# Performance work log

Measured on AMD Instinct MI355X. Metric: run time of the kernel, lower is better.

## Reference

```python
import jax, jax.numpy as jnp
import numpy as np


def grid_sample_bilinear(img, grid):
    """Replicates torch F.grid_sample(mode='bilinear', padding_mode='zeros',
    align_corners=False). img: [B,C,Hin,Win]; grid: [B,Ho,Wo,2] in [-1,1]
    with grid[...,0]=x (width), grid[...,1]=y (height). Returns [B,C,Ho,Wo]."""
    B, C, Hin, Win = img.shape
    x = (grid[..., 0] + 1.0) * (Win * 0.5) - 0.5  # unnormalized pixel coords
    y = (grid[..., 1] + 1.0) * (Hin * 0.5) - 0.5
    x0 = jnp.floor(x)
    y0 = jnp.floor(y)
    wx1 = x - x0
    wy1 = y - y0

    def tap(xi, yi, w):
        valid = ((xi >= 0) & (xi < Win) & (yi >= 0) & (yi < Hin)).astype(img.dtype)
        xc = jnp.clip(xi, 0, Win - 1).astype(jnp.int32)
        yc = jnp.clip(yi, 0, Hin - 1).astype(jnp.int32)
        def gather_one(im, yb, xb, wb):
            return im[:, yb, xb] * wb[None]  # [C,Ho,Wo]
        return jax.vmap(gather_one)(img, yc, xc, valid * w)

    return (tap(x0, y0, (1.0 - wx1) * (1.0 - wy1))
            + tap(x0 + 1.0, y0, wx1 * (1.0 - wy1))
            + tap(x0, y0 + 1.0, (1.0 - wx1) * wy1)
            + tap(x0 + 1.0, y0 + 1.0, wx1 * wy1))


def setup_inputs() -> dict:
    key = jax.random.key(0)
    k_uv, k1, k2, k3, k4 = jax.random.split(key, 5)
    W, H = 2048, 2048
    B, Ho, Wo = 8, 1024, 1024
    return {
        "uv": jax.random.uniform(k_uv, (B, Ho, Wo, 2), dtype=jnp.float32),
        "layer1": jax.random.normal(k1, (1, 1, W, H), dtype=jnp.float32),
        "layer2": jax.random.normal(k2, (1, 1, W // 2, H // 2), dtype=jnp.float32),
        "layer3": jax.random.normal(k3, (1, 1, W // 4, H // 4), dtype=jnp.float32),
        "layer4": jax.random.normal(k4, (1, 1, W // 8, H // 8), dtype=jnp.float32),
    }


def reference(uv, layer1, layer2, layer3, layer4):
    B = uv.shape[0]
    grid = uv * 2.0 - 1.0
    y = None
    for layer in (layer1, layer2, layer3, layer4):
        img = jnp.broadcast_to(layer, (B,) + layer.shape[1:])  # repeat(B,1,1,1)
        s = grid_sample_bilinear(img, grid)
        y = s if y is None else y + s
    return y  # [B,1,Ho,Wo]
```

## Files before the change

kernel.cpp:

```cpp
#include <hip/hip_runtime.h>
#include <hip/hip_fp16.h>


typedef unsigned int u32x2 __attribute__((ext_vector_type(2)));
typedef float f32x4 __attribute__((ext_vector_type(4)));

#define K 1024
#define CHUNK 4096
#define HB 4096
#define SEG (CHUNK * 256)
#define NXCD 8

__device__ __forceinline__ int binof(float u, float v) {
    int bx = min(max((int)(u * 32.0f), 0), 31);
    int by = min(max((int)(v * 32.0f), 0), 31);
    return by * 32 + bx;
}

__global__ __launch_bounds__(256) void repack_hist_kernel(
    const float* __restrict__ l1, const float* __restrict__ l2,
    const float* __restrict__ l3, const float* __restrict__ l4,
    __half2* __restrict__ r1, __half2* __restrict__ r2,
    __half2* __restrict__ r3, __half2* __restrict__ r4,
    const float2* __restrict__ uv, unsigned* __restrict__ hist, int n) {
    const int n1 = 2048 * 2048, n2 = 1024 * 1024, n3 = 512 * 512, n4 = 256 * 256;
    int i = blockIdx.x * 256 + threadIdx.x;
    {
        const float* __restrict__ src = nullptr;
        __half2* __restrict__ dst = nullptr;
        int S = 0, logS = 0, j = 0;
        if (i < n1) {
            src = l1; dst = r1; S = 2048; logS = 11; j = i;
        } else if (i < n1 + n2) {
            src = l2; dst = r2; S = 1024; logS = 10; j = i - n1;
        } else if (i < n1 + n2 + n3) {
            src = l3; dst = r3; S = 512; logS = 9; j = i - (n1 + n2);
        } else if (i < n1 + n2 + n3 + n4) {
            src = l4; dst = r4; S = 256; logS = 8; j = i - (n1 + n2 + n3);
        }
        if (src) {
            int y = j >> logS;
            float a = src[j];
            float b = src[(y < S - 1) ? (j + S) : j];
            dst[j] = __halves2half2(__float2half(a), __float2half(b));
        }
    }
    if (hist == nullptr) return;
    int base = blockIdx.x * HB;
    if (base >= n) return;
    __shared__ unsigned cnt[K];
    for (int b = threadIdx.x; b < K; b += 256) cnt[b] = 0u;
    __syncthreads();
    int m = min(HB, n - base);
    const f32x4* uv4 = (const f32x4*)(uv + base);
    int npair = m >> 1;
    for (int k2 = threadIdx.x; k2 < npair; k2 += 256) {
        f32x4 q = __builtin_nontemporal_load(&uv4[k2]);
        atomicAdd(&cnt[binof(q.x, q.y)], 1u);
        atomicAdd(&cnt[binof(q.z, q.w)], 1u);
    }
    if ((m & 1) && threadIdx.x == 0) {
        float2 q = uv[base + m - 1];
        atomicAdd(&cnt[binof(q.x, q.y)], 1u);
    }
    __syncthreads();
    int seg = base / SEG;
    unsigned* gh = hist + (size_t)seg * K;
    for (int b = threadIdx.x; b < K; b += 256) {
        unsigned v = cnt[b];
        if (v) atomicAdd(&gh[b], v);
    }
}

__global__ __launch_bounds__(256) void partition_kernel(
    const float2* __restrict__ uv, const unsigned* __restrict__ hist,
    unsigned* __restrict__ cursor, float2* __restrict__ uv_s,
    unsigned* __restrict__ idx_s, int n, int pinned) {
    __shared__ float2 suv[CHUNK];
    __shared__ unsigned short slid[CHUNK];
    __shared__ unsigned cnt[K];
    __shared__ unsigned lbase[K];
    __shared__ unsigned goff[K];
    __shared__ unsigned part[256];
    int t = threadIdx.x;
    int blk = blockIdx.x;
    int c = pinned ? ((blk % NXCD) * (SEG / CHUNK) + blk / NXCD) : blk;
    int cb = c * CHUNK;
    if (cb >= n) return;
    int cnum = min(CHUNK, n - cb);
    int seg = cb / SEG;
    unsigned segstart = (unsigned)((size_t)seg * SEG);

    {
        const f32x4* uv4 = (const f32x4*)(uv + cb);
        int npair = cnum >> 1;
        for (int k2 = t; k2 < npair; k2 += 256) {
            f32x4 q = uv4[k2];
            suv[k2 * 2] = make_float2(q.x, q.y);
            suv[k2 * 2 + 1] = make_float2(q.z, q.w);
        }
        if ((cnum & 1) && t == 0) suv[cnum - 1] = uv[cb + cnum - 1];
    }
    for (int b = t; b < K; b += 256) cnt[b] = 0u;
    __syncthreads();
    for (int k = t; k < cnum; k += 256)
        atomicAdd(&cnt[binof(suv[k].x, suv[k].y)], 1u);
    __syncthreads();
    {
        unsigned v0 = cnt[t * 4], v1 = cnt[t * 4 + 1], v2 = cnt[t * 4 + 2],
                 v3 = cnt[t * 4 + 3];
        unsigned s1 = v0, s2 = v0 + v1, s3 = v0 + v1 + v2;
        part[t] = s3 + v3;
        __syncthreads();
        for (int off = 1; off < 256; off <<= 1) {
            unsigned x = (t >= off) ? part[t - off] : 0u;
            __syncthreads();
            part[t] += x;
            __syncthreads();
        }
        unsigned tb = (t > 0) ? part[t - 1] : 0u;
        lbase[t * 4] = tb;
        lbase[t * 4 + 1] = tb + s1;
        lbase[t * 4 + 2] = tb + s2;
        lbase[t * 4 + 3] = tb + s3;
    }
    __syncthreads();
    {
        const unsigned* h = hist + (size_t)seg * K;
        unsigned v0 = h[t * 4], v1 = h[t * 4 + 1], v2 = h[t * 4 + 2],
                 v3 = h[t * 4 + 3];
        unsigned s1 = v0, s2 = v0 + v1, s3 = v0 + v1 + v2;
        part[t] = s3 + v3;
        __syncthreads();
        for (int off = 1; off < 256; off <<= 1) {
            unsigned x = (t >= off) ? part[t - off] : 0u;
            __syncthreads();
            part[t] += x;
            __syncthreads();
        }
        unsigned tb = (t > 0) ? part[t - 1] : 0u;
        unsigned sbv[4] = {tb, tb + s1, tb + s2, tb + s3};
        for (int j = 0; j < 4; ++j) {
            int b = t * 4 + j;
            unsigned cc = cnt[b];
            unsigned r = cc ? atomicAdd(&cursor[(size_t)seg * K + b], cc) : 0u;
            goff[b] = segstart + sbv[j] + r;
        }
    }
    __syncthreads();
    for (int b = t; b < K; b += 256) cnt[b] = 0u;
    __syncthreads();
    for (int k = t; k < cnum; k += 256) {
        int b = binof(suv[k].x, suv[k].y);
        unsigned r = lbase[b] + atomicAdd(&cnt[b], 1u);
        slid[r] = (unsigned short)k;
    }
    __syncthreads();
    for (int s = t; s < cnum; s += 256) {
        int lid = slid[s];
        float2 q = suv[lid];
        int b = binof(q.x, q.y);
        unsigned pos = goff[b] + ((unsigned)s - lbase[b]);
        uv_s[pos] = q;
        idx_s[pos] = (unsigned)(cb + lid);
    }
}

__device__ __forceinline__ float sample_level(const __half2* __restrict__ R,
                                              const int S, const float gx,
                                              const float gy) {
    const float halfS = 0.5f * (float)S;
    float x = (gx + 1.0f) * halfS - 0.5f;
    float y = (gy + 1.0f) * halfS - 0.5f;
    float xf = floorf(x), yf = floorf(y);
    float wx = x - xf, wy = y - yf;
    int x0 = (int)xf, y0 = (int)yf;

    int yc = min(max(y0, 0), S - 1);
    float wa = (y0 >= 0) ? (1.0f - wy) : wy;
    if (y0 < -1 || y0 >= S) wa = 0.0f;
    float wb = (y0 >= 0 && y0 < S - 1) ? wy : 0.0f;

    int xb = min(max(x0, 0), S - 2);
    bool xin = (x0 >= 0) && (x0 <= S - 2);
    float wxa = xin ? (1.0f - wx) : ((x0 == -1) ? wx : 0.0f);
    float wxb = xin ? wx : ((x0 == S - 1) ? (1.0f - wx) : 0.0f);

    uint2 q;
    __builtin_memcpy(&q, (const char*)(R + (size_t)yc * (size_t)S + xb), 8);
    __half2 ca = *(const __half2*)&q.x;
    __half2 cb = *(const __half2*)&q.y;
    float2 fa = __half22float2(ca);
    float2 fb = __half22float2(cb);
    float cola = fmaf(wa, fa.x, wb * fa.y);
    float colb = fmaf(wa, fb.x, wb * fb.y);
    return fmaf(wxa, cola, wxb * colb);
}

__device__ __forceinline__ float sample_point(const __half2* __restrict__ r1,
                                              const __half2* __restrict__ r2,
                                              const __half2* __restrict__ r3,
                                              const __half2* __restrict__ r4,
                                              float ux, float uy) {
    float gx = ux * 2.0f - 1.0f;
    float gy = uy * 2.0f - 1.0f;
    float acc = sample_level(r1, 2048, gx, gy);
    acc += sample_level(r2, 1024, gx, gy);
    acc += sample_level(r3, 512, gx, gy);
    acc += sample_level(r4, 256, gx, gy);
    return acc;
}

__global__ __launch_bounds__(256) void lappyr_sample_sorted(
    const float2* __restrict__ uv_s, const unsigned* __restrict__ idx_s,
    const __half2* __restrict__ r1, const __half2* __restrict__ r2,
    const __half2* __restrict__ r3, const __half2* __restrict__ r4,
    float* __restrict__ out, int n, int pinned) {
    int blk = blockIdx.x;
    int sb = pinned ? ((blk % NXCD) * (SEG / 512) + blk / NXCD) : blk;
    int i = sb * 256 + threadIdx.x;
    int p0 = i * 2;
    if (p0 >= n) return;
    if (p0 + 1 < n) {
        f32x4 q = __builtin_nontemporal_load((const f32x4*)uv_s + i);
        u32x2 id = __builtin_nontemporal_load((const u32x2*)idx_s + i);
        float a0 = sample_point(r1, r2, r3, r4, q.x, q.y);
        float a1 = sample_point(r1, r2, r3, r4, q.z, q.w);
        out[id.x] = a0;
        out[id.y] = a1;
    } else {
        float2 q = uv_s[p0];
        out[idx_s[p0]] = sample_point(r1, r2, r3, r4, q.x, q.y);
    }
}

__global__ __launch_bounds__(256) void lappyr_sample_kernel(
    const float2* __restrict__ uv, const __half2* __restrict__ r1,
    const __half2* __restrict__ r2, const __half2* __restrict__ r3,
    const __half2* __restrict__ r4, float* __restrict__ out, int n) {
    int i = blockIdx.x * blockDim.x + threadIdx.x;
    if (i >= n) return;
    float2 p = uv[i];
    out[i] = sample_point(r1, r2, r3, r4, p.x, p.y);
}

__device__ __forceinline__ float bilin_f32(const float* __restrict__ img,
                                           const int S, const float gx,
                                           const float gy) {
    const float halfS = 0.5f * (float)S;
    float x = (gx + 1.0f) * halfS - 0.5f;
    float y = (gy + 1.0f) * halfS - 0.5f;
    float xf = floorf(x), yf = floorf(y);
    float wx = x - xf, wy = y - yf;
    int x0 = (int)xf, y0 = (int)yf, x1 = x0 + 1, y1 = y0 + 1;
    float ex0 = (x0 >= 0 && x0 < S) ? (1.0f - wx) : 0.0f;
    float ex1 = (x1 >= 0 && x1 < S) ? wx : 0.0f;
    float ey0 = (y0 >= 0 && y0 < S) ? (1.0f - wy) : 0.0f;
    float ey1 = (y1 >= 0 && y1 < S) ? wy : 0.0f;
    int xc0 = min(max(x0, 0), S - 1), xc1 = min(max(x1, 0), S - 1);
    int yc0 = min(max(y0, 0), S - 1), yc1 = min(max(y1, 0), S - 1);
    const float* r0 = img + (size_t)yc0 * S;
    const float* r1 = img + (size_t)yc1 * S;
    return ey0 * fmaf(ex0, r0[xc0], ex1 * r0[xc1]) +
           ey1 * fmaf(ex0, r1[xc0], ex1 * r1[xc1]);
}

__global__ __launch_bounds__(256) void lappyr_f32_kernel(
    const float2* __restrict__ uv, const float* __restrict__ l1,
    const float* __restrict__ l2, const float* __restrict__ l3,
    const float* __restrict__ l4, float* __restrict__ out, int n) {
    int i = blockIdx.x * blockDim.x + threadIdx.x;
    if (i >= n) return;
    float2 p = uv[i];
    float gx = p.x * 2.0f - 1.0f;
    float gy = p.y * 2.0f - 1.0f;
    float acc = bilin_f32(l1, 2048, gx, gy);
    acc += bilin_f32(l2, 1024, gx, gy);
    acc += bilin_f32(l3, 512, gx, gy);
    acc += bilin_f32(l4, 256, gx, gy);
    out[i] = acc;
}

extern "C" void kernel_launch(void* const* d_in, const int* in_sizes, int n_in,
                              void* d_out, int out_size, void* d_ws, size_t ws_size,
                              hipStream_t stream) {
    const float2* uv = (const float2*)d_in[0];
    const float* l1 = (const float*)d_in[1];
    const float* l2 = (const float*)d_in[2];
    const float* l3 = (const float*)d_in[3];
    const float* l4 = (const float*)d_in[4];
    float* out = (float*)d_out;
    int n = out_size;

    const size_t n1 = 2048u * 2048u, n2 = 1024u * 1024u, n3 = 512u * 512u,
                 n4 = 256u * 256u;
    const size_t ntot = n1 + n2 + n3 + n4;
    const size_t rep_bytes = ntot * sizeof(__half2);

    int nseg = (n + SEG - 1) / SEG;
    size_t off_uvs = (rep_bytes + 255) & ~(size_t)255;
    size_t off_idx = off_uvs + (size_t)n * 8;
    size_t off_hist = (off_idx + (size_t)n * 4 + 255) & ~(size_t)255;
    size_t off_cur = off_hist + (size_t)nseg * K * 4;
    size_t need_sort = off_cur + (size_t)nseg * K * 4;

    int repack_blocks = (int)((ntot + 255) / 256);

    if (ws_size >= rep_bytes) {
        char* ws = (char*)d_ws;
        __half2* r1 = (__half2*)ws;
        __half2* r2 = r1 + n1;
        __half2* r3 = r2 + n2;
        __half2* r4 = r3 + n3;
        bool do_sort = (ws_size >= need_sort) && (n > 0);
        if (do_sort) {
            float2* uv_s = (float2*)(ws + off_uvs);
            unsigned* idx_s = (unsigned*)(ws + off_idx);
            unsigned* hist = (unsigned*)(ws + off_hist);
            unsigned* cursor = (unsigned*)(ws + off_cur);
            int pinned = (n == NXCD * SEG) ? 1 : 0;
            hipMemsetAsync(ws + off_hist, 0, (size_t)nseg * K * 4 * 2, stream);
            int hist_blocks = (n + HB - 1) / HB;
            int ga = max(repack_blocks, hist_blocks);
            repack_hist_kernel<<<ga, 256, 0, stream>>>(l1, l2, l3, l4, r1, r2, r3,
                                                       r4, uv, hist, n);
            int nchunks = (n + CHUNK - 1) / CHUNK;
            partition_kernel<<<nchunks, 256, 0, stream>>>(uv, hist, cursor, uv_s,
                                                          idx_s, n, pinned);
            int nh = (n + 1) / 2;
            lappyr_sample_sorted<<<(nh + 255) / 256, 256, 0, stream>>>(
                uv_s, idx_s, r1, r2, r3, r4, out, n, pinned);
        } else {
            repack_hist_kernel<<<repack_blocks, 256, 0, stream>>>(
                l1, l2, l3, l4, r1, r2, r3, r4, uv, nullptr, n);
            lappyr_sample_kernel<<<(n + 255) / 256, 256, 0, stream>>>(
                uv, r1, r2, r3, r4, out, n);
        }
    } else {
        lappyr_f32_kernel<<<(n + 255) / 256, 256, 0, stream>>>(uv, l1, l2, l3, l4,
                                                               out, n);
    }
}
```

Baseline: 361.1 us.

## Replace scattered output writes with sorted values plus inverse-permutation gather pass

Partition now records an inverse permutation (the sorted position of each original point) instead of the sorted-to-original index. Sampling writes its results contiguously in sorted order, and a separate unsort kernel gathers them back using the inverse permutation, so output writes are coalesced. This swaps scattered 4-byte stores for scattered 4-byte loads, at the cost of an extra kernel launch and an extra intermediate buffer that must be written and read. The old path is kept as a fallback when the workspace is too small.

```diff
diff --git a/kernel.cpp b/kernel.cpp
--- a/kernel.cpp
+++ b/kernel.cpp
@@ -3,6 +3,7 @@
 
 
 typedef unsigned int u32x2 __attribute__((ext_vector_type(2)));
+typedef unsigned int u32x4 __attribute__((ext_vector_type(4)));
 typedef float f32x4 __attribute__((ext_vector_type(4)));
 
 #define K 1024
@@ -75,7 +76,8 @@
 __global__ __launch_bounds__(256) void partition_kernel(
     const float2* __restrict__ uv, const unsigned* __restrict__ hist,
     unsigned* __restrict__ cursor, float2* __restrict__ uv_s,
-    unsigned* __restrict__ idx_s, int n, int pinned) {
+    unsigned* __restrict__ invp, unsigned* __restrict__ idxp, int n,
+    int pinned) {
     __shared__ float2 suv[CHUNK];
     __shared__ unsigned short slid[CHUNK];
     __shared__ unsigned cnt[K];
@@ -152,8 +154,9 @@
     __syncthreads();
     for (int k = t; k < cnum; k += 256) {
         int b = binof(suv[k].x, suv[k].y);
-        unsigned r = lbase[b] + atomicAdd(&cnt[b], 1u);
-        slid[r] = (unsigned short)k;
+        unsigned r = atomicAdd(&cnt[b], 1u);
+        slid[lbase[b] + r] = (unsigned short)k;
+        if (invp) invp[cb + k] = goff[b] + r;
     }
     __syncthreads();
     for (int s = t; s < cnum; s += 256) {
@@ -162,7 +165,7 @@
         int b = binof(q.x, q.y);
         unsigned pos = goff[b] + ((unsigned)s - lbase[b]);
         uv_s[pos] = q;
-        idx_s[pos] = (unsigned)(cb + lid);
+        if (idxp) idxp[pos] = (unsigned)(cb + lid);
     }
 }
 
@@ -209,6 +212,57 @@
     acc += sample_level(r3, 512, gx, gy);
     acc += sample_level(r4, 256, gx, gy);
     return acc;
+}
+
+__global__ __launch_bounds__(256) void lappyr_sample4(
+    const float2* __restrict__ uv_s, const __half2* __restrict__ r1,
+    const __half2* __restrict__ r2, const __half2* __restrict__ r3,
+    const __half2* __restrict__ r4, float* __restrict__ val_s, int n,
+    int pinned) {
+    int blk = blockIdx.x;
+    int sb = pinned ? ((blk % NXCD) * (SEG / 1024) + blk / NXCD) : blk;
+    int base = sb * 1024 + threadIdx.x * 4;
+    if (base + 3 < n) {
+        const f32x4* u4 = (const f32x4*)(uv_s + base);
+        f32x4 a = __builtin_nontemporal_load(u4);
+        f32x4 b = __builtin_nontemporal_load(u4 + 1);
+        f32x4 res;
+        res.x = sample_point(r1, r2, r3, r4, a.x, a.y);
+        res.y = sample_point(r1, r2, r3, r4, a.z, a.w);
+        res.z = sample_point(r1, r2, r3, r4, b.x, b.y);
+        res.w = sample_point(r1, r2, r3, r4, b.z, b.w);
+        *(f32x4*)(val_s + base) = res;
+    } else {
+        for (int j = 0; j < 4; ++j) {
+            int p = base + j;
+            if (p < n) {
+                float2 q = uv_s[p];
+                val_s[p] = sample_point(r1, r2, r3, r4, q.x, q.y);
+            }
+        }
+    }
+}
+
+__global__ __launch_bounds__(256) void lappyr_unsort4(
+    const unsigned* __restrict__ inv, const float* __restrict__ val_s,
+    float* __restrict__ out, int n, int pinned) {
+    int blk = blockIdx.x;
+    int sb = pinned ? ((blk % NXCD) * (SEG / 1024) + blk / NXCD) : blk;
+    int base = sb * 1024 + threadIdx.x * 4;
+    if (base + 3 < n) {
+        u32x4 iv = __builtin_nontemporal_load((const u32x4*)(inv + base));
+        f32x4 res;
+        res.x = val_s[iv.x];
+        res.y = val_s[iv.y];
+        res.z = val_s[iv.z];
+        res.w = val_s[iv.w];
+        __builtin_nontemporal_store(res, (f32x4*)(out + base));
+    } else {
+        for (int j = 0; j < 4; ++j) {
+            int p = base + j;
+            if (p < n) out[p] = val_s[inv[p]];
+        }
+    }
 }
 
 __global__ __launch_bounds__(256) void lappyr_sample_sorted(
@@ -298,11 +352,16 @@
     const size_t rep_bytes = ntot * sizeof(__half2);
 
     int nseg = (n + SEG - 1) / SEG;
+    size_t tbl_bytes = (size_t)nseg * K * 4 * 2;
+
     size_t off_uvs = (rep_bytes + 255) & ~(size_t)255;
+    size_t off_inv = off_uvs + (size_t)n * 8;
+    size_t off_val = off_inv + (size_t)n * 4;
+    size_t off_hist2 = (off_val + (size_t)n * 4 + 255) & ~(size_t)255;
+    size_t need2 = off_hist2 + tbl_bytes;
     size_t off_idx = off_uvs + (size_t)n * 8;
-    size_t off_hist = (off_idx + (size_t)n * 4 + 255) & ~(size_t)255;
-    size_t off_cur = off_hist + (size_t)nseg * K * 4;
-    size_t need_sort = off_cur + (size_t)nseg * K * 4;
+    size_t off_hist1 = (off_idx + (size_t)n * 4 + 255) & ~(size_t)255;
+    size_t need1 = off_hist1 + tbl_bytes;
 
     int repack_blocks = (int)((ntot + 255) / 256);
 
@@ -312,21 +371,35 @@
         __half2* r2 = r1 + n1;
         __half2* r3 = r2 + n2;
         __half2* r4 = r3 + n3;
-        bool do_sort = (ws_size >= need_sort) && (n > 0);
-        if (do_sort) {
+        int pinned = (n == NXCD * SEG) ? 1 : 0;
+        int hist_blocks = (n + HB - 1) / HB;
+        int ga = max(repack_blocks, hist_blocks);
+        int nchunks = (n + CHUNK - 1) / CHUNK;
+        if (ws_size >= need2 && n > 0) {
+            float2* uv_s = (float2*)(ws + off_uvs);
+            unsigned* inv = (unsigned*)(ws + off_inv);
+            float* val_s = (float*)(ws + off_val);
+            unsigned* hist = (unsigned*)(ws + off_hist2);
+            unsigned* cursor = hist + (size_t)nseg * K;
+            hipMemsetAsync(ws + off_hist2, 0, tbl_bytes, stream);
+            repack_hist_kernel<<<ga, 256, 0, stream>>>(l1, l2, l3, l4, r1, r2, r3,
+                                                       r4, uv, hist, n);
+            partition_kernel<<<nchunks, 256, 0, stream>>>(
+                uv, hist, cursor, uv_s, inv, nullptr, n, pinned);
+            int nb4 = (n + 1023) / 1024;
+            lappyr_sample4<<<nb4, 256, 0, stream>>>(uv_s, r1, r2, r3, r4, val_s,
+                                                    n, pinned);
+            lappyr_unsort4<<<nb4, 256, 0, stream>>>(inv, val_s, out, n, pinned);
+        } else if (ws_size >= need1 && n > 0) {
             float2* uv_s = (float2*)(ws + off_uvs);
             unsigned* idx_s = (unsigned*)(ws + off_idx);
-            unsigned* hist = (unsigned*)(ws + off_hist);
-            unsigned* cursor = (unsigned*)(ws + off_cur);
-            int pinned = (n == NXCD * SEG) ? 1 : 0;
-            hipMemsetAsync(ws + off_hist, 0, (size_t)nseg * K * 4 * 2, stream);
-            int hist_blocks = (n + HB - 1) / HB;
-            int ga = max(repack_blocks, hist_blocks);
+            unsigned* hist = (unsigned*)(ws + off_hist1);
+            unsigned* cursor = hist + (size_t)nseg * K;
+            hipMemsetAsync(ws + off_hist1, 0, tbl_bytes, stream);
             repack_hist_kernel<<<ga, 256, 0, stream>>>(l1, l2, l3, l4, r1, r2, r3,
                                                        r4, uv, hist, n);
-            int nchunks = (n + CHUNK - 1) / CHUNK;
-            partition_kernel<<<nchunks, 256, 0, stream>>>(uv, hist, cursor, uv_s,
-                                                          idx_s, n, pinned);
+            partition_kernel<<<nchunks, 256, 0, stream>>>(
+                uv, hist, cursor, uv_s, nullptr, idx_s, n, pinned);
             int nh = (n + 1) / 2;
             lappyr_sample_sorted<<<(nh + 255) / 256, 256, 0, stream>>>(
                 uv_s, idx_s, r1, r2, r3, r4, out, n, pinned);
```

New measurement: 312.5 us. 13.5% less time.
